# Kernel tuning notes

Measured on AMD Instinct MI355X. Metric: run time of the kernel, lower is better.

The kernel has to match this reference:

```python
import jax, jax.numpy as jnp
import numpy as np

MAXLEN = (270 * 270 + 480 * 480) / 4.0  # 75825.0


def setup_inputs() -> dict:
    key = jax.random.key(0)
    k1, k2 = jax.random.split(key)
    shape = (64, 3, 17, 4096)  # (bs, ddim=3, actionlen, seqlen)
    predict = jax.random.normal(k1, shape, dtype=jnp.float32)
    target = jax.random.normal(k2, shape, dtype=jnp.float32)
    return {"predict": predict, "target": target}


def reference(predict, target):
    bs, ddim, actionlen, seqlen = predict.shape
    # per-channel weights: channels 0,1 weight 1, channel 2 weight MAXLEN
    w = jnp.asarray([1.0, 1.0, MAXLEN], dtype=predict.dtype)
    sq = (target - predict) ** 2  # [bs, 3, actionlen, seqlen]
    total = jnp.sum(sq * w[None, :, None, None])
    return total / (bs * seqlen * actionlen)
```

## Files before the change

kernel.cpp:

```cpp
#include <hip/hip_runtime.h>


#define BLOCK_SIZE 256
#define ITERS 8
#define VEC_PER_CHAN 17408
#define W2 75825.0f

__device__ __forceinline__ float blockReduce(float acc, float* smem) {
    for (int off = 32; off > 0; off >>= 1)
        acc += __shfl_down(acc, off, 64);
    const int lane = threadIdx.x & 63;
    const int wid = threadIdx.x >> 6;
    if (lane == 0) smem[wid] = acc;
    __syncthreads();
    float s = 0.0f;
    if (threadIdx.x == 0) {
        #pragma unroll
        for (int w = 0; w < BLOCK_SIZE / 64; ++w) s += smem[w];
    }
    return s;
}

__global__ __launch_bounds__(BLOCK_SIZE) void pm_mse_partial_exact(
    const float4* __restrict__ p, const float4* __restrict__ t,
    float* __restrict__ partial, int stride ) {
    const int tid = blockIdx.x * BLOCK_SIZE + threadIdx.x;

    float4 a[ITERS], b[ITERS];
    #pragma unroll
    for (int k = 0; k < ITERS; ++k) {
        int i = tid + k * stride;
        a[k] = p[i];
        b[k] = t[i];
    }
    float acc = 0.0f;
    #pragma unroll
    for (int k = 0; k < ITERS; ++k) {
        int i = tid + k * stride;
        float dx = b[k].x - a[k].x;
        float dy = b[k].y - a[k].y;
        float dz = b[k].z - a[k].z;
        float dw = b[k].w - a[k].w;
        float s = dx * dx + dy * dy + dz * dz + dw * dw;
        int c = (i / VEC_PER_CHAN) % 3;
        acc += (c == 2) ? s * W2 : s;
    }

    __shared__ float smem[BLOCK_SIZE / 64];
    float s = blockReduce(acc, smem);
    if (threadIdx.x == 0) partial[blockIdx.x] = s;
}

__global__ __launch_bounds__(BLOCK_SIZE) void pm_mse_partial_generic(
    const float4* __restrict__ p, const float4* __restrict__ t,
    float* __restrict__ partial, int n4) {
    float acc = 0.0f;
    const int stride = gridDim.x * blockDim.x;
    for (int i = blockIdx.x * blockDim.x + threadIdx.x; i < n4; i += stride) {
        float4 a = p[i];
        float4 b = t[i];
        float dx = b.x - a.x;
        float dy = b.y - a.y;
        float dz = b.z - a.z;
        float dw = b.w - a.w;
        float s = dx * dx + dy * dy + dz * dz + dw * dw;
        int c = (i / VEC_PER_CHAN) % 3;
        acc += (c == 2) ? s * W2 : s;
    }
    __shared__ float smem[BLOCK_SIZE / 64];
    float s = blockReduce(acc, smem);
    if (threadIdx.x == 0) partial[blockIdx.x] = s;
}

__global__ __launch_bounds__(BLOCK_SIZE) void pm_mse_final(
    const float* __restrict__ partial, int nblocks, float* __restrict__ out,
    float scale) {
    double acc = 0.0;
    for (int i = threadIdx.x; i < nblocks; i += blockDim.x)
        acc += (double)partial[i];
    for (int off = 32; off > 0; off >>= 1)
        acc += __shfl_down(acc, off, 64);
    __shared__ double smem[BLOCK_SIZE / 64];
    const int lane = threadIdx.x & 63;
    const int wid = threadIdx.x >> 6;
    if (lane == 0) smem[wid] = acc;
    __syncthreads();
    if (threadIdx.x == 0) {
        double s = 0.0;
        #pragma unroll
        for (int w = 0; w < BLOCK_SIZE / 64; ++w) s += smem[w];
        out[0] = (float)(s * (double)scale);
    }
}

extern "C" void kernel_launch(void* const* d_in, const int* in_sizes, int n_in,
                              void* d_out, int out_size, void* d_ws, size_t ws_size,
                              hipStream_t stream) {
    const float* predict = (const float*)d_in[0];
    const float* target  = (const float*)d_in[1];
    float* out = (float*)d_out;
    float* partial = (float*)d_ws;

    const int n = in_sizes[0];
    const int n4 = n / 4;
    const float scale = 3.0f / (float)n;

    const int chunk = BLOCK_SIZE * ITERS;
    if (n4 % chunk == 0) {
        const int blocks = n4 / chunk;
        const int stride = blocks * BLOCK_SIZE;
        pm_mse_partial_exact<<<blocks, BLOCK_SIZE, 0, stream>>>(
            (const float4*)predict, (const float4*)target, partial, stride);
        pm_mse_final<<<1, BLOCK_SIZE, 0, stream>>>(partial, blocks, out, scale);
    } else {
        int blocks = (n4 + BLOCK_SIZE - 1) / BLOCK_SIZE;
        if (blocks > 2048) blocks = 2048;
        pm_mse_partial_generic<<<blocks, BLOCK_SIZE, 0, stream>>>(
            (const float4*)predict, (const float4*)target, partial, n4);
        pm_mse_final<<<1, BLOCK_SIZE, 0, stream>>>(partial, blocks, out, scale);
    }
}
```

Baseline: 121.9 us.

## Fuse final reduction into main kernel via last-block atomic counter

Replaces the separate final-reduction kernel with a last-block-done pattern: each block writes its partial sum, increments an atomic counter, and the last block reduces all partials in double precision. A memset resets the counter before each launch. It also lowers per-thread loads from 8 to 3 float4 pairs, which increases the block count. This adds an atomic per block and a memset operation, and it relies on the workspace being large enough.

Result: slower. 312.8 us (+156.6%).

```diff
diff --git a/kernel.cpp b/kernel.cpp
--- a/kernel.cpp
+++ b/kernel.cpp
@@ -2,15 +2,17 @@
 
 
 #define BLOCK_SIZE 256
-#define ITERS 8
+#define ITERS 3
 #define VEC_PER_CHAN 17408
 #define W2 75825.0f
+#define PARTIAL_OFF 64
 
-__device__ __forceinline__ float blockReduce(float acc, float* smem) {
+__device__ __forceinline__ float blockReduceF(float acc, float* smem) {
+    #pragma unroll
     for (int off = 32; off > 0; off >>= 1)
         acc += __shfl_down(acc, off, 64);
     const int lane = threadIdx.x & 63;
-    const int wid = threadIdx.x >> 6;
+    const int wid  = threadIdx.x >> 6;
     if (lane == 0) smem[wid] = acc;
     __syncthreads();
     float s = 0.0f;
@@ -21,34 +23,66 @@
     return s;
 }
 
-__global__ __launch_bounds__(BLOCK_SIZE) void pm_mse_partial_exact(
+__global__ __launch_bounds__(BLOCK_SIZE) void pm_mse_fused(
     const float4* __restrict__ p, const float4* __restrict__ t,
-    float* __restrict__ partial, int stride ) {
+    float* __restrict__ ws, float* __restrict__ out,
+    int stride , int nblocks, float scale) {
     const int tid = blockIdx.x * BLOCK_SIZE + threadIdx.x;
 
     float4 a[ITERS], b[ITERS];
     #pragma unroll
     for (int k = 0; k < ITERS; ++k) {
-        int i = tid + k * stride;
+        const int i = tid + k * stride;
         a[k] = p[i];
         b[k] = t[i];
     }
     float acc = 0.0f;
     #pragma unroll
     for (int k = 0; k < ITERS; ++k) {
-        int i = tid + k * stride;
+        const int i = tid + k * stride;
         float dx = b[k].x - a[k].x;
         float dy = b[k].y - a[k].y;
         float dz = b[k].z - a[k].z;
         float dw = b[k].w - a[k].w;
         float s = dx * dx + dy * dy + dz * dz + dw * dw;
-        int c = (i / VEC_PER_CHAN) % 3;
+        const int c = (i / VEC_PER_CHAN) % 3;
         acc += (c == 2) ? s * W2 : s;
     }
 
     __shared__ float smem[BLOCK_SIZE / 64];
-    float s = blockReduce(acc, smem);
-    if (threadIdx.x == 0) partial[blockIdx.x] = s;
+    float s = blockReduceF(acc, smem);
+
+    unsigned int* counter = (unsigned int*)ws;
+    float* partial = ws + PARTIAL_OFF;
+
+    __shared__ bool amLast;
+    if (threadIdx.x == 0) {
+        partial[blockIdx.x] = s;
+        __threadfence();
+        const unsigned int prev = atomicAdd(counter, 1u);
+        amLast = (prev == (unsigned int)(nblocks - 1));
+    }
+    __syncthreads();
+    if (!amLast) return;
+
+    __threadfence();
+    double dacc = 0.0;
+    for (int i = threadIdx.x; i < nblocks; i += BLOCK_SIZE)
+        dacc += (double)partial[i];
+    #pragma unroll
+    for (int off = 32; off > 0; off >>= 1)
+        dacc += __shfl_down(dacc, off, 64);
+    __shared__ double dsm[BLOCK_SIZE / 64];
+    const int lane = threadIdx.x & 63;
+    const int wid  = threadIdx.x >> 6;
+    if (lane == 0) dsm[wid] = dacc;
+    __syncthreads();
+    if (threadIdx.x == 0) {
+        double tot = 0.0;
+        #pragma unroll
+        for (int w = 0; w < BLOCK_SIZE / 64; ++w) tot += dsm[w];
+        out[0] = (float)(tot * (double)scale);
+    }
 }
 
 __global__ __launch_bounds__(BLOCK_SIZE) void pm_mse_partial_generic(
@@ -68,7 +102,7 @@
         acc += (c == 2) ? s * W2 : s;
     }
     __shared__ float smem[BLOCK_SIZE / 64];
-    float s = blockReduce(acc, smem);
+    float s = blockReduceF(acc, smem);
     if (threadIdx.x == 0) partial[blockIdx.x] = s;
 }
 
@@ -99,24 +133,25 @@
     const float* predict = (const float*)d_in[0];
     const float* target  = (const float*)d_in[1];
     float* out = (float*)d_out;
-    float* partial = (float*)d_ws;
+    float* ws = (float*)d_ws;
 
     const int n = in_sizes[0];
     const int n4 = n / 4;
     const float scale = 3.0f / (float)n;
 
     const int chunk = BLOCK_SIZE * ITERS;
-    if (n4 % chunk == 0) {
+    if (n4 % chunk == 0 && (size_t)ws_size >= (PARTIAL_OFF + (size_t)(n4 / chunk)) * 4) {
         const int blocks = n4 / chunk;
         const int stride = blocks * BLOCK_SIZE;
-        pm_mse_partial_exact<<<blocks, BLOCK_SIZE, 0, stream>>>(
-            (const float4*)predict, (const float4*)target, partial, stride);
-        pm_mse_final<<<1, BLOCK_SIZE, 0, stream>>>(partial, blocks, out, scale);
+        hipMemsetAsync(d_ws, 0, sizeof(unsigned int), stream);
+        pm_mse_fused<<<blocks, BLOCK_SIZE, 0, stream>>>(
+            (const float4*)predict, (const float4*)target, ws, out,
+            stride, blocks, scale);
     } else {
         int blocks = (n4 + BLOCK_SIZE - 1) / BLOCK_SIZE;
         if (blocks > 2048) blocks = 2048;
         pm_mse_partial_generic<<<blocks, BLOCK_SIZE, 0, stream>>>(
-            (const float4*)predict, (const float4*)target, partial, n4);
-        pm_mse_final<<<1, BLOCK_SIZE, 0, stream>>>(partial, blocks, out, scale);
+            (const float4*)predict, (const float4*)target, ws + PARTIAL_OFF, n4);
+        pm_mse_final<<<1, BLOCK_SIZE, 0, stream>>>(ws + PARTIAL_OFF, blocks, out, scale);
     }
 }
```
